# Kernel optimization log

Hardware: AMD Instinct MI355X
Metric: run time of the kernel (lower is better)

The kernel has to match this reference:

```python
import jax, jax.numpy as jnp
import numpy as np

def setup_inputs() -> dict:
    key = jax.random.key(0)
    ks = jax.random.split(key, 6)
    ch, cr = 256, 32  # cr = ch // 8
    B, H, W = 4, 64, 64
    sc = 1.0 / np.sqrt(ch)
    return {
        "inputs": jax.random.normal(ks[0], (B, H, W, ch), jnp.float32),
        "Wf": jax.random.normal(ks[1], (ch, cr), jnp.float32) * sc,
        "bf": jnp.zeros((cr,), jnp.float32),
        "Wg": jax.random.normal(ks[2], (ch, cr), jnp.float32) * sc,
        "bg": jnp.zeros((cr,), jnp.float32),
        "Wh": jax.random.normal(ks[3], (ch, cr), jnp.float32) * sc,
        "bh": jnp.zeros((cr,), jnp.float32),
        "Wv": jax.random.normal(ks[4], (cr, ch), jnp.float32) * (1.0 / np.sqrt(cr)),
        "bv": jnp.zeros((ch,), jnp.float32),
        "gamma": jnp.zeros((1,), jnp.float32),
    }

def reference(inputs, Wf, bf, Wg, bg, Wh, bh, Wv, bv, gamma):
    B, H, W, C = inputs.shape
    x = inputs.reshape(B, H * W, C)  # [B, N, C]
    f = x @ Wf + bf  # [B, N, cr] (keys)
    g = x @ Wg + bg  # [B, N, cr] (queries)
    h = x @ Wh + bh  # [B, N, cr] (values)
    s = jnp.einsum('bnk,bmk->bnm', g, f)  # [B, N, N]
    beta = jax.nn.softmax(s, axis=-1)
    v = jnp.einsum('bnm,bmk->bnk', beta, h)  # [B, N, cr]
    o = v @ Wv + bv  # [B, N, C]
    out = gamma * o + x
    return out.reshape(B, H, W, C)
```

## Files before the change

### kernel.cpp

```cpp
#include <hip/hip_runtime.h>

#define B_SZ  4
#define N_TOK 4096
#define CH    256
#define CR    32
#define SEG   512
#define KT    64
#define NITER (SEG / KT)
#define SHIFT 12.0f

typedef __attribute__((ext_vector_type(8))) short bf16x8;
typedef __attribute__((ext_vector_type(4))) float f32x4;

__device__ inline ushort f2bf(float x) {
    uint u = __float_as_uint(x);
    u += 0x7fff + ((u >> 16) & 1);
    return (ushort)(u >> 16);
}
__device__ inline uint pk2bf(float a, float b) {
    return __builtin_amdgcn_perm(__float_as_uint(b), __float_as_uint(a), 0x07060302);
}

__global__ __launch_bounds__(256) void prep_kernel(
    const float* __restrict__ Wf, const float* __restrict__ Wg,
    const float* __restrict__ Wh, const float* __restrict__ Wv,
    ushort* __restrict__ wft, ushort* __restrict__ wgt,
    ushort* __restrict__ wht, ushort* __restrict__ wvt)
{
    int t = threadIdx.x, blk = blockIdx.x;
    if (blk < 3) {
        const float* W  = (blk == 0) ? Wf : (blk == 1) ? Wg : Wh;
        ushort*      Wt = (blk == 0) ? wft : (blk == 1) ? wgt : wht;
        int j = t & 31, half = t >> 5;
        ushort tmp[32];
        #pragma unroll
        for (int kk = 0; kk < 32; ++kk)
            tmp[kk] = f2bf(W[(half * 32 + kk) * CR + j]);
        ushort* dst = Wt + (size_t)j * CH + half * 32;
        #pragma unroll
        for (int k8 = 0; k8 < 4; ++k8)
            *(bf16x8*)(dst + k8 * 8) = *(bf16x8*)&tmp[k8 * 8];
    } else {
        ushort tmp[32];
        #pragma unroll
        for (int k = 0; k < CR; ++k) tmp[k] = f2bf(Wv[k * CH + t]);
        ushort* dst = wvt + (size_t)t * CR;
        #pragma unroll
        for (int k8 = 0; k8 < 4; ++k8)
            *(bf16x8*)(dst + k8 * 8) = *(bf16x8*)&tmp[k8 * 8];
    }
}

__global__ __launch_bounds__(256) void proj_kernel(
    const float* __restrict__ x,
    const ushort* __restrict__ wft, const ushort* __restrict__ wgt, const ushort* __restrict__ wht,
    const float* __restrict__ bf_, const float* __restrict__ bg, const float* __restrict__ bh,
    ushort* __restrict__ fo, ushort* __restrict__ go, ushort* __restrict__ hto)
{
    __shared__ f32x4 accx[3][6][64];
    int t  = threadIdx.x;
    int wv = t >> 6, L = t & 63, nl = L & 15, Q = L >> 4;
    int row_t = blockIdx.x * 16;
    int b = row_t >> 12, tok0 = row_t & 4095;

    const float* xrow = x + (size_t)(row_t + nl) * CH;
    f32x4 A[6];
    #pragma unroll
    for (int i = 0; i < 6; ++i) A[i] = (f32x4){0.f, 0.f, 0.f, 0.f};

    #pragma unroll
    for (int c2 = 0; c2 < 2; ++c2) {
        int off = wv * 64 + c2 * 32 + Q * 8;
        float4 lo = *(const float4*)(xrow + off);
        float4 hi = *(const float4*)(xrow + off + 4);
        bf16x8 xa;
        xa[0] = (short)f2bf(lo.x); xa[1] = (short)f2bf(lo.y);
        xa[2] = (short)f2bf(lo.z); xa[3] = (short)f2bf(lo.w);
        xa[4] = (short)f2bf(hi.x); xa[5] = (short)f2bf(hi.y);
        xa[6] = (short)f2bf(hi.z); xa[7] = (short)f2bf(hi.w);

        bf16x8 wf0 = *(const bf16x8*)(wft + (size_t)nl * CH + off);
        bf16x8 wf1 = *(const bf16x8*)(wft + (size_t)(16 + nl) * CH + off);
        bf16x8 wg0 = *(const bf16x8*)(wgt + (size_t)nl * CH + off);
        bf16x8 wg1 = *(const bf16x8*)(wgt + (size_t)(16 + nl) * CH + off);
        bf16x8 wh0 = *(const bf16x8*)(wht + (size_t)nl * CH + off);
        bf16x8 wh1 = *(const bf16x8*)(wht + (size_t)(16 + nl) * CH + off);

        A[0] = __builtin_amdgcn_mfma_f32_16x16x32_bf16(xa, wf0, A[0], 0, 0, 0);
        A[1] = __builtin_amdgcn_mfma_f32_16x16x32_bf16(xa, wf1, A[1], 0, 0, 0);
        A[2] = __builtin_amdgcn_mfma_f32_16x16x32_bf16(xa, wg0, A[2], 0, 0, 0);
        A[3] = __builtin_amdgcn_mfma_f32_16x16x32_bf16(xa, wg1, A[3], 0, 0, 0);
        A[4] = __builtin_amdgcn_mfma_f32_16x16x32_bf16(wh0, xa, A[4], 0, 0, 0);
        A[5] = __builtin_amdgcn_mfma_f32_16x16x32_bf16(wh1, xa, A[5], 0, 0, 0);
    }

    if (wv > 0) {
        #pragma unroll
        for (int i = 0; i < 6; ++i) accx[wv - 1][i][L] = A[i];
    }
    __syncthreads();
    if (wv == 0) {
        #pragma unroll
        for (int i = 0; i < 6; ++i) {
            f32x4 s0 = accx[0][i][L], s1 = accx[1][i][L], s2 = accx[2][i][L];
            A[i] = A[i] + s0 + s1 + s2;
        }
        float bF0 = bf_[nl], bF1 = bf_[16 + nl];
        float bG0 = bg[nl],  bG1 = bg[16 + nl];
        #pragma unroll
        for (int r = 0; r < 4; ++r) {
            size_t ro = (size_t)(row_t + Q * 4 + r) * CR;
            fo[ro + nl]      = f2bf(A[0][r] + bF0);
            fo[ro + 16 + nl] = f2bf(A[1][r] + bF1);
            go[ro + nl]      = f2bf(A[2][r] + bG0);
            go[ro + 16 + nl] = f2bf(A[3][r] + bG1);
        }
        ushort* hb = hto + (size_t)b * CR * N_TOK + tok0 + nl;
        #pragma unroll
        for (int r = 0; r < 4; ++r) {
            int ch = Q * 4 + r;
            hb[(size_t)ch * N_TOK]        = f2bf(A[4][r] + bh[ch]);
            hb[(size_t)(16 + ch) * N_TOK] = f2bf(A[5][r] + bh[16 + ch]);
        }
    }
}

__global__ __launch_bounds__(512, 4) void attn_kernel(
    const ushort* __restrict__ f, const ushort* __restrict__ g,
    const ushort* __restrict__ ht, const ushort* __restrict__ wvt,
    const float* __restrict__ bv, const float* __restrict__ gamma,
    const float* __restrict__ x, float* __restrict__ out)
{
    __shared__ unsigned long long smem_raw[38912 / 8];
    ushort (*pls)[32][76]  = (ushort (*)[32][76])smem_raw;
    float  (*obuf)[32][33] = (float (*)[32][33])smem_raw;
    float  (*lbuf)[32]     = (float (*)[32])((char*)smem_raw + 33792);
    ushort (*oc)[48]       = (ushort (*)[48])((char*)smem_raw + 34816);

    int t  = threadIdx.x;
    int wv = t >> 6;
    int L  = t & 63;
    int nl = L & 15;
    int Q  = L >> 4;
    int b  = blockIdx.x >> 7;
    int q0 = (blockIdx.x & 127) * 32;

    const ushort* fb  = f  + (size_t)b * N_TOK * CR;
    const ushort* htb = ht + (size_t)b * CR * N_TOK;

    bf16x8 gB0 = *(const bf16x8*)(g + ((size_t)b * N_TOK + q0 + nl) * CR + Q * 8);
    bf16x8 gB1 = *(const bf16x8*)(g + ((size_t)b * N_TOK + q0 + 16 + nl) * CR + Q * 8);

    f32x4 acc00 = {0,0,0,0}, acc01 = {0,0,0,0};
    f32x4 acc10 = {0,0,0,0}, acc11 = {0,0,0,0};
    const f32x4 zf = {0,0,0,0};
    float lsum0 = 0.f, lsum1 = 0.f;

    int key0 = wv * SEG;
    bf16x8 Ac0 = *(const bf16x8*)(fb + (size_t)(key0 +  0 + nl) * CR + Q * 8);
    bf16x8 Ac1 = *(const bf16x8*)(fb + (size_t)(key0 + 16 + nl) * CR + Q * 8);
    bf16x8 Ac2 = *(const bf16x8*)(fb + (size_t)(key0 + 32 + nl) * CR + Q * 8);
    bf16x8 Ac3 = *(const bf16x8*)(fb + (size_t)(key0 + 48 + nl) * CR + Q * 8);

    #pragma unroll 2
    for (int it = 0; it < NITER; ++it) {
        int kc = wv * SEG + it * KT;
        const ushort* hk = htb + (size_t)nl * N_TOK + kc;
        bf16x8 b00 = *(const bf16x8*)(hk + Q * 8);
        bf16x8 b01 = *(const bf16x8*)(hk + (size_t)16 * N_TOK + Q * 8);
        bf16x8 b10 = *(const bf16x8*)(hk + 32 + Q * 8);
        bf16x8 b11 = *(const bf16x8*)(hk + (size_t)16 * N_TOK + 32 + Q * 8);
        int kn = wv * SEG + ((it + 1 < NITER) ? it + 1 : 0) * KT;
        const ushort* fn = fb + (size_t)kn * CR;
        bf16x8 An0 = *(const bf16x8*)(fn + (size_t)( 0 + nl) * CR + Q * 8);
        bf16x8 An1 = *(const bf16x8*)(fn + (size_t)(16 + nl) * CR + Q * 8);
        bf16x8 An2 = *(const bf16x8*)(fn + (size_t)(32 + nl) * CR + Q * 8);
        bf16x8 An3 = *(const bf16x8*)(fn + (size_t)(48 + nl) * CR + Q * 8);

        f32x4 s00 = __builtin_amdgcn_mfma_f32_16x16x32_bf16(Ac0, gB0, zf, 0, 0, 0);
        f32x4 s01 = __builtin_amdgcn_mfma_f32_16x16x32_bf16(Ac1, gB0, zf, 0, 0, 0);
        f32x4 s02 = __builtin_amdgcn_mfma_f32_16x16x32_bf16(Ac2, gB0, zf, 0, 0, 0);
        f32x4 s03 = __builtin_amdgcn_mfma_f32_16x16x32_bf16(Ac3, gB0, zf, 0, 0, 0);
        f32x4 s10 = __builtin_amdgcn_mfma_f32_16x16x32_bf16(Ac0, gB1, zf, 0, 0, 0);
        f32x4 s11 = __builtin_amdgcn_mfma_f32_16x16x32_bf16(Ac1, gB1, zf, 0, 0, 0);
        f32x4 s12 = __builtin_amdgcn_mfma_f32_16x16x32_bf16(Ac2, gB1, zf, 0, 0, 0);
        f32x4 s13 = __builtin_amdgcn_mfma_f32_16x16x32_bf16(Ac3, gB1, zf, 0, 0, 0);

        #pragma unroll
        for (int qh = 0; qh < 2; ++qh) {
            f32x4 v0 = qh ? s10 : s00, v1 = qh ? s11 : s01;
            f32x4 v2 = qh ? s12 : s02, v3 = qh ? s13 : s03;
            int row = qh * 16 + nl;
            float p0 = __expf(v0[0]-SHIFT), p1 = __expf(v0[1]-SHIFT), p2 = __expf(v0[2]-SHIFT), p3 = __expf(v0[3]-SHIFT);
            float s4 = ((p0+p1)+(p2+p3));
            uint2 w; w.x = pk2bf(p0,p1); w.y = pk2bf(p2,p3);
            *(uint2*)&pls[wv][row][ 0 + Q * 4] = w;
            p0 = __expf(v1[0]-SHIFT); p1 = __expf(v1[1]-SHIFT); p2 = __expf(v1[2]-SHIFT); p3 = __expf(v1[3]-SHIFT);
            s4 += ((p0+p1)+(p2+p3));
            w.x = pk2bf(p0,p1); w.y = pk2bf(p2,p3);
            *(uint2*)&pls[wv][row][16 + Q * 4] = w;
            p0 = __expf(v2[0]-SHIFT); p1 = __expf(v2[1]-SHIFT); p2 = __expf(v2[2]-SHIFT); p3 = __expf(v2[3]-SHIFT);
            s4 += ((p0+p1)+(p2+p3));
            w.x = pk2bf(p0,p1); w.y = pk2bf(p2,p3);
            *(uint2*)&pls[wv][row][32 + Q * 4] = w;
            p0 = __expf(v3[0]-SHIFT); p1 = __expf(v3[1]-SHIFT); p2 = __expf(v3[2]-SHIFT); p3 = __expf(v3[3]-SHIFT);
            s4 += ((p0+p1)+(p2+p3));
            w.x = pk2bf(p0,p1); w.y = pk2bf(p2,p3);
            *(uint2*)&pls[wv][row][48 + Q * 4] = w;
            if (qh) lsum1 += s4; else lsum0 += s4;
        }

        bf16x8 aP00 = *(const bf16x8*)&pls[wv][     nl][ 0 + Q * 8];
        bf16x8 aP01 = *(const bf16x8*)&pls[wv][     nl][32 + Q * 8];
        bf16x8 aP10 = *(const bf16x8*)&pls[wv][16 + nl][ 0 + Q * 8];
        bf16x8 aP11 = *(const bf16x8*)&pls[wv][16 + nl][32 + Q * 8];

        acc00 = __builtin_amdgcn_mfma_f32_16x16x32_bf16(aP00, b00, acc00, 0, 0, 0);
        acc01 = __builtin_amdgcn_mfma_f32_16x16x32_bf16(aP00, b01, acc01, 0, 0, 0);
        acc10 = __builtin_amdgcn_mfma_f32_16x16x32_bf16(aP10, b00, acc10, 0, 0, 0);
        acc11 = __builtin_amdgcn_mfma_f32_16x16x32_bf16(aP10, b01, acc11, 0, 0, 0);
        acc00 = __builtin_amdgcn_mfma_f32_16x16x32_bf16(aP01, b10, acc00, 0, 0, 0);
        acc01 = __builtin_amdgcn_mfma_f32_16x16x32_bf16(aP01, b11, acc01, 0, 0, 0);
        acc10 = __builtin_amdgcn_mfma_f32_16x16x32_bf16(aP11, b10, acc10, 0, 0, 0);
        acc11 = __builtin_amdgcn_mfma_f32_16x16x32_bf16(aP11, b11, acc11, 0, 0, 0);

        Ac0 = An0; Ac1 = An1; Ac2 = An2; Ac3 = An3;
    }

    lsum0 += __shfl_xor(lsum0, 16); lsum0 += __shfl_xor(lsum0, 32);
    lsum1 += __shfl_xor(lsum1, 16); lsum1 += __shfl_xor(lsum1, 32);

    __syncthreads();
    #pragma unroll
    for (int r = 0; r < 4; ++r) {
        obuf[wv][     Q * 4 + r][nl]      = acc00[r];
        obuf[wv][     Q * 4 + r][16 + nl] = acc01[r];
        obuf[wv][16 + Q * 4 + r][nl]      = acc10[r];
        obuf[wv][16 + Q * 4 + r][16 + nl] = acc11[r];
    }
    if (L < 16) { lbuf[wv][nl] = lsum0; lbuf[wv][16 + nl] = lsum1; }
    __syncthreads();

    {
        int ch = t & 31, qb = t >> 5;
        #pragma unroll
        for (int qq = qb; qq < 32; qq += 16) {
            float s = 0.f, Lq = 0.f;
            #pragma unroll
            for (int w = 0; w < 8; ++w) { s += obuf[w][qq][ch]; Lq += lbuf[w][qq]; }
            oc[qq][ch] = f2bf(s / Lq);
        }
    }
    __syncthreads();

    bf16x8 aO0 = *(const bf16x8*)&oc[     nl][Q * 8];
    bf16x8 aO1 = *(const bf16x8*)&oc[16 + nl][Q * 8];
    float gm = gamma[0];
    const float* xb = x   + ((size_t)b * N_TOK + q0) * CH;
    float*       ob = out + ((size_t)b * N_TOK + q0) * CH;
    #pragma unroll
    for (int i = 0; i < 2; ++i) {
        int nb = wv * 2 + i;
        bf16x8 bW = *(const bf16x8*)(wvt + (size_t)(nb * 16 + nl) * CR + Q * 8);
        f32x4 d0 = __builtin_amdgcn_mfma_f32_16x16x32_bf16(aO0, bW, zf, 0, 0, 0);
        f32x4 d1 = __builtin_amdgcn_mfma_f32_16x16x32_bf16(aO1, bW, zf, 0, 0, 0);
        int c = nb * 16 + nl;
        float bvc = bv[c];
        #pragma unroll
        for (int r = 0; r < 4; ++r) {
            int qa = Q * 4 + r;
            ob[qa * CH + c]        = fmaf(gm, d0[r] + bvc, xb[qa * CH + c]);
            ob[(16 + qa) * CH + c] = fmaf(gm, d1[r] + bvc, xb[(16 + qa) * CH + c]);
        }
    }
}

extern "C" void kernel_launch(void* const* d_in, const int* in_sizes, int n_in,
                              void* d_out, int out_size, void* d_ws, size_t ws_size,
                              hipStream_t stream) {
    const float* x     = (const float*)d_in[0];
    const float* Wf    = (const float*)d_in[1];
    const float* bf_   = (const float*)d_in[2];
    const float* Wg    = (const float*)d_in[3];
    const float* bg    = (const float*)d_in[4];
    const float* Wh    = (const float*)d_in[5];
    const float* bh    = (const float*)d_in[6];
    const float* Wv    = (const float*)d_in[7];
    const float* bv    = (const float*)d_in[8];
    const float* gamma = (const float*)d_in[9];
    float* out = (float*)d_out;

    const size_t T = (size_t)B_SZ * N_TOK * CR;
    ushort* fo  = (ushort*)d_ws;
    ushort* go  = fo + T;
    ushort* hto = go + T;
    ushort* wvt = hto + T;
    ushort* wft = wvt + CH * CR;
    ushort* wgt = wft + CH * CR;
    ushort* wht = wgt + CH * CR;

    prep_kernel<<<4, 256, 0, stream>>>(Wf, Wg, Wh, Wv, wft, wgt, wht, wvt);
    proj_kernel<<<B_SZ * N_TOK / 16, 256, 0, stream>>>(x, wft, wgt, wht, bf_, bg, bh, fo, go, hto);
    attn_kernel<<<B_SZ * (N_TOK / 32), 512, 0, stream>>>(fo, go, hto, wvt, bv, gamma, x, out);
}
```

Baseline: 122.3 us.

## Fold log2e into queries, use exp2, widen key tile and drop register prefetch

The query projection is pre-scaled by log2(e), so the softmax exponent becomes a plain exp2 with a pre-scaled shift and no per-element multiply. The key tile grows from 64 to 128, processed as two 64-key sub-steps, with all K and V fragments loaded at the top of each iteration instead of prefetched one iteration ahead. Launch bounds are relaxed from 4 to 2 blocks per CU to allow more registers, at the cost of fewer resident waves and less latency hiding. Rounding the log2e-scaled g to bf16 slightly changes numerics.

```diff
diff --git a/kernel.cpp b/kernel.cpp
--- a/kernel.cpp
+++ b/kernel.cpp
@@ -5,9 +5,10 @@
 #define CH    256
 #define CR    32
 #define SEG   512
-#define KT    64
+#define KT    128
 #define NITER (SEG / KT)
-#define SHIFT 12.0f
+#define LOG2E 1.44269504f
+#define SHIFT2 (12.0f * 1.44269504f)
 
 typedef __attribute__((ext_vector_type(8))) short bf16x8;
 typedef __attribute__((ext_vector_type(4))) float f32x4;
@@ -106,14 +107,14 @@
             A[i] = A[i] + s0 + s1 + s2;
         }
         float bF0 = bf_[nl], bF1 = bf_[16 + nl];
-        float bG0 = bg[nl],  bG1 = bg[16 + nl];
+        float bG0 = bg[nl] * LOG2E, bG1 = bg[16 + nl] * LOG2E;
         #pragma unroll
         for (int r = 0; r < 4; ++r) {
             size_t ro = (size_t)(row_t + Q * 4 + r) * CR;
             fo[ro + nl]      = f2bf(A[0][r] + bF0);
             fo[ro + 16 + nl] = f2bf(A[1][r] + bF1);
-            go[ro + nl]      = f2bf(A[2][r] + bG0);
-            go[ro + 16 + nl] = f2bf(A[3][r] + bG1);
+            go[ro + nl]      = f2bf(fmaf(A[2][r], LOG2E, bG0));
+            go[ro + 16 + nl] = f2bf(fmaf(A[3][r], LOG2E, bG1));
         }
         ushort* hb = hto + (size_t)b * CR * N_TOK + tok0 + nl;
         #pragma unroll
@@ -125,7 +126,7 @@
     }
 }
 
-__global__ __launch_bounds__(512, 4) void attn_kernel(
+__global__ __launch_bounds__(512, 2) void attn_kernel(
     const ushort* __restrict__ f, const ushort* __restrict__ g,
     const ushort* __restrict__ ht, const ushort* __restrict__ wvt,
     const float* __restrict__ bv, const float* __restrict__ gamma,
@@ -156,75 +157,60 @@
     const f32x4 zf = {0,0,0,0};
     float lsum0 = 0.f, lsum1 = 0.f;
 
-    int key0 = wv * SEG;
-    bf16x8 Ac0 = *(const bf16x8*)(fb + (size_t)(key0 +  0 + nl) * CR + Q * 8);
-    bf16x8 Ac1 = *(const bf16x8*)(fb + (size_t)(key0 + 16 + nl) * CR + Q * 8);
-    bf16x8 Ac2 = *(const bf16x8*)(fb + (size_t)(key0 + 32 + nl) * CR + Q * 8);
-    bf16x8 Ac3 = *(const bf16x8*)(fb + (size_t)(key0 + 48 + nl) * CR + Q * 8);
-
-    #pragma unroll 2
+    #pragma unroll 1
     for (int it = 0; it < NITER; ++it) {
         int kc = wv * SEG + it * KT;
+        const ushort* fk = fb + (size_t)kc * CR;
+        bf16x8 A[8];
+        #pragma unroll
+        for (int sk = 0; sk < 8; ++sk)
+            A[sk] = *(const bf16x8*)(fk + (size_t)(sk * 16 + nl) * CR + Q * 8);
         const ushort* hk = htb + (size_t)nl * N_TOK + kc;
-        bf16x8 b00 = *(const bf16x8*)(hk + Q * 8);
-        bf16x8 b01 = *(const bf16x8*)(hk + (size_t)16 * N_TOK + Q * 8);
-        bf16x8 b10 = *(const bf16x8*)(hk + 32 + Q * 8);
-        bf16x8 b11 = *(const bf16x8*)(hk + (size_t)16 * N_TOK + 32 + Q * 8);
-        int kn = wv * SEG + ((it + 1 < NITER) ? it + 1 : 0) * KT;
-        const ushort* fn = fb + (size_t)kn * CR;
-        bf16x8 An0 = *(const bf16x8*)(fn + (size_t)( 0 + nl) * CR + Q * 8);
-        bf16x8 An1 = *(const bf16x8*)(fn + (size_t)(16 + nl) * CR + Q * 8);
-        bf16x8 An2 = *(const bf16x8*)(fn + (size_t)(32 + nl) * CR + Q * 8);
-        bf16x8 An3 = *(const bf16x8*)(fn + (size_t)(48 + nl) * CR + Q * 8);
-
-        f32x4 s00 = __builtin_amdgcn_mfma_f32_16x16x32_bf16(Ac0, gB0, zf, 0, 0, 0);
-        f32x4 s01 = __builtin_amdgcn_mfma_f32_16x16x32_bf16(Ac1, gB0, zf, 0, 0, 0);
-        f32x4 s02 = __builtin_amdgcn_mfma_f32_16x16x32_bf16(Ac2, gB0, zf, 0, 0, 0);
-        f32x4 s03 = __builtin_amdgcn_mfma_f32_16x16x32_bf16(Ac3, gB0, zf, 0, 0, 0);
-        f32x4 s10 = __builtin_amdgcn_mfma_f32_16x16x32_bf16(Ac0, gB1, zf, 0, 0, 0);
-        f32x4 s11 = __builtin_amdgcn_mfma_f32_16x16x32_bf16(Ac1, gB1, zf, 0, 0, 0);
-        f32x4 s12 = __builtin_amdgcn_mfma_f32_16x16x32_bf16(Ac2, gB1, zf, 0, 0, 0);
-        f32x4 s13 = __builtin_amdgcn_mfma_f32_16x16x32_bf16(Ac3, gB1, zf, 0, 0, 0);
-
-        #pragma unroll
-        for (int qh = 0; qh < 2; ++qh) {
-            f32x4 v0 = qh ? s10 : s00, v1 = qh ? s11 : s01;
-            f32x4 v2 = qh ? s12 : s02, v3 = qh ? s13 : s03;
-            int row = qh * 16 + nl;
-            float p0 = __expf(v0[0]-SHIFT), p1 = __expf(v0[1]-SHIFT), p2 = __expf(v0[2]-SHIFT), p3 = __expf(v0[3]-SHIFT);
-            float s4 = ((p0+p1)+(p2+p3));
-            uint2 w; w.x = pk2bf(p0,p1); w.y = pk2bf(p2,p3);
-            *(uint2*)&pls[wv][row][ 0 + Q * 4] = w;
-            p0 = __expf(v1[0]-SHIFT); p1 = __expf(v1[1]-SHIFT); p2 = __expf(v1[2]-SHIFT); p3 = __expf(v1[3]-SHIFT);
-            s4 += ((p0+p1)+(p2+p3));
-            w.x = pk2bf(p0,p1); w.y = pk2bf(p2,p3);
-            *(uint2*)&pls[wv][row][16 + Q * 4] = w;
-            p0 = __expf(v2[0]-SHIFT); p1 = __expf(v2[1]-SHIFT); p2 = __expf(v2[2]-SHIFT); p3 = __expf(v2[3]-SHIFT);
-            s4 += ((p0+p1)+(p2+p3));
-            w.x = pk2bf(p0,p1); w.y = pk2bf(p2,p3);
-            *(uint2*)&pls[wv][row][32 + Q * 4] = w;
-            p0 = __expf(v3[0]-SHIFT); p1 = __expf(v3[1]-SHIFT); p2 = __expf(v3[2]-SHIFT); p3 = __expf(v3[3]-SHIFT);
-            s4 += ((p0+p1)+(p2+p3));
-            w.x = pk2bf(p0,p1); w.y = pk2bf(p2,p3);
-            *(uint2*)&pls[wv][row][48 + Q * 4] = w;
-            if (qh) lsum1 += s4; else lsum0 += s4;
-        }
-
-        bf16x8 aP00 = *(const bf16x8*)&pls[wv][     nl][ 0 + Q * 8];
-        bf16x8 aP01 = *(const bf16x8*)&pls[wv][     nl][32 + Q * 8];
-        bf16x8 aP10 = *(const bf16x8*)&pls[wv][16 + nl][ 0 + Q * 8];
-        bf16x8 aP11 = *(const bf16x8*)&pls[wv][16 + nl][32 + Q * 8];
-
-        acc00 = __builtin_amdgcn_mfma_f32_16x16x32_bf16(aP00, b00, acc00, 0, 0, 0);
-        acc01 = __builtin_amdgcn_mfma_f32_16x16x32_bf16(aP00, b01, acc01, 0, 0, 0);
-        acc10 = __builtin_amdgcn_mfma_f32_16x16x32_bf16(aP10, b00, acc10, 0, 0, 0);
-        acc11 = __builtin_amdgcn_mfma_f32_16x16x32_bf16(aP10, b01, acc11, 0, 0, 0);
-        acc00 = __builtin_amdgcn_mfma_f32_16x16x32_bf16(aP01, b10, acc00, 0, 0, 0);
-        acc01 = __builtin_amdgcn_mfma_f32_16x16x32_bf16(aP01, b11, acc01, 0, 0, 0);
-        acc10 = __builtin_amdgcn_mfma_f32_16x16x32_bf16(aP11, b10, acc10, 0, 0, 0);
-        acc11 = __builtin_amdgcn_mfma_f32_16x16x32_bf16(aP11, b11, acc11, 0, 0, 0);
-
-        Ac0 = An0; Ac1 = An1; Ac2 = An2; Ac3 = An3;
+        bf16x8 Bv[8];
+        #pragma unroll
+        for (int kq = 0; kq < 4; ++kq) {
+            Bv[kq * 2 + 0] = *(const bf16x8*)(hk + kq * 32 + Q * 8);
+            Bv[kq * 2 + 1] = *(const bf16x8*)(hk + (size_t)16 * N_TOK + kq * 32 + Q * 8);
+        }
+
+        f32x4 S0[8], S1[8];
+        #pragma unroll
+        for (int sk = 0; sk < 8; ++sk) {
+            S0[sk] = __builtin_amdgcn_mfma_f32_16x16x32_bf16(A[sk], gB0, zf, 0, 0, 0);
+            S1[sk] = __builtin_amdgcn_mfma_f32_16x16x32_bf16(A[sk], gB1, zf, 0, 0, 0);
+        }
+
+        #pragma unroll
+        for (int sub = 0; sub < 2; ++sub) {
+            #pragma unroll
+            for (int qh = 0; qh < 2; ++qh) {
+                int row = qh * 16 + nl;
+                float s4 = 0.f;
+                #pragma unroll
+                for (int j = 0; j < 4; ++j) {
+                    f32x4 sv = qh ? S1[sub * 4 + j] : S0[sub * 4 + j];
+                    float p0 = exp2f(sv[0] - SHIFT2), p1 = exp2f(sv[1] - SHIFT2);
+                    float p2 = exp2f(sv[2] - SHIFT2), p3 = exp2f(sv[3] - SHIFT2);
+                    s4 += (p0 + p1) + (p2 + p3);
+                    uint2 w; w.x = pk2bf(p0, p1); w.y = pk2bf(p2, p3);
+                    *(uint2*)&pls[wv][row][j * 16 + Q * 4] = w;
+                }
+                if (qh) lsum1 += s4; else lsum0 += s4;
+            }
+            bf16x8 aP00 = *(const bf16x8*)&pls[wv][     nl][ 0 + Q * 8];
+            bf16x8 aP01 = *(const bf16x8*)&pls[wv][     nl][32 + Q * 8];
+            bf16x8 aP10 = *(const bf16x8*)&pls[wv][16 + nl][ 0 + Q * 8];
+            bf16x8 aP11 = *(const bf16x8*)&pls[wv][16 + nl][32 + Q * 8];
+
+            acc00 = __builtin_amdgcn_mfma_f32_16x16x32_bf16(aP00, Bv[sub * 4 + 0], acc00, 0, 0, 0);
+            acc01 = __builtin_amdgcn_mfma_f32_16x16x32_bf16(aP00, Bv[sub * 4 + 1], acc01, 0, 0, 0);
+            acc10 = __builtin_amdgcn_mfma_f32_16x16x32_bf16(aP10, Bv[sub * 4 + 0], acc10, 0, 0, 0);
+            acc11 = __builtin_amdgcn_mfma_f32_16x16x32_bf16(aP10, Bv[sub * 4 + 1], acc11, 0, 0, 0);
+            acc00 = __builtin_amdgcn_mfma_f32_16x16x32_bf16(aP01, Bv[sub * 4 + 2], acc00, 0, 0, 0);
+            acc01 = __builtin_amdgcn_mfma_f32_16x16x32_bf16(aP01, Bv[sub * 4 + 3], acc01, 0, 0, 0);
+            acc10 = __builtin_amdgcn_mfma_f32_16x16x32_bf16(aP11, Bv[sub * 4 + 2], acc10, 0, 0, 0);
+            acc11 = __builtin_amdgcn_mfma_f32_16x16x32_bf16(aP11, Bv[sub * 4 + 3], acc11, 0, 0, 0);
+        }
     }
 
     lsum0 += __shfl_xor(lsum0, 16); lsum0 += __shfl_xor(lsum0, 32);
```

Result: slower. 127.6 us (+4.3%).
